# Kernel tuning notes

Measured on AMD Instinct MI355X. Metric: run time of the kernel, lower is better.

Reference implementation:

```python
import jax, jax.numpy as jnp
import numpy as np

K = 256      # embedding size k
STATE = 128  # latent state size
IN = 64      # external input size
OBS = 64     # observation size
L = 512      # sequence length (time-major)
B = 256      # batch size


def _glorot(key, shape):
    return jax.random.normal(key, shape, dtype=jnp.float32) / float(np.sqrt(shape[0]))


def setup_inputs():
    key = jax.random.key(0)
    ks = jax.random.split(key, 12)
    p = {}
    p["external_input_seq"] = jax.random.normal(ks[0], (L, B, IN), dtype=jnp.float32)
    p["observations_seq"] = jax.random.normal(ks[1], (L, B, OBS), dtype=jnp.float32)
    p["eps"] = jax.random.normal(ks[2], (L, B, STATE), dtype=jnp.float32)  # reparam noise
    # PreProcess: Linear + tanh
    p["Wu"] = _glorot(ks[3], (IN, K)); p["bu"] = jnp.zeros((K,), jnp.float32)
    p["Wx"] = _glorot(ks[4], (OBS, K)); p["bx"] = jnp.zeros((K,), jnp.float32)
    # input_rnn: vanilla tanh RNN, 1 layer, k -> k
    p["W_ih"] = _glorot(ks[5], (K, K)); p["b_ih"] = jnp.zeros((K,), jnp.float32)
    p["W_hh"] = _glorot(ks[6], (K, K)); p["b_hh"] = jnp.zeros((K,), jnp.float32)
    # posterior_a_layer: MLP(2k, k, k, 1) = Linear -> tanh -> Linear
    p["Wa1"] = _glorot(ks[7], (2 * K, K)); p["ba1"] = jnp.zeros((K,), jnp.float32)
    p["Wa2"] = _glorot(ks[8], (K, K)); p["ba2"] = jnp.zeros((K,), jnp.float32)

    def dblock_params(k1, in_dim, hid, out):
        kk = jax.random.split(k1, 4)
        return (_glorot(kk[0], (in_dim, hid)), jnp.zeros((hid,), jnp.float32),
                _glorot(kk[1], (in_dim, hid)), jnp.zeros((hid,), jnp.float32),
                _glorot(kk[2], (hid, out)), jnp.zeros((out,), jnp.float32),
                _glorot(kk[3], (hid, out)), jnp.zeros((out,), jnp.float32))

    names = ["f1_W", "f1_b", "f2_W", "f2_b", "mu_W", "mu_b", "ls_W", "ls_b"]
    for pref, kk in (("post_", ks[9]), ("prior_", ks[10])):
        vals = dblock_params(kk, STATE + K, 2 * K, STATE)
        for n, v in zip(names, vals):
            p[pref + n] = v
    return p


def _dblock(x, f1_W, f1_b, f2_W, f2_b, mu_W, mu_b, ls_W, ls_b):
    # TD-VAE DBlock: gated hidden, then mu / logsigma heads
    t = jnp.tanh(x @ f1_W + f1_b) * jax.nn.sigmoid(x @ f2_W + f2_b)
    return t @ mu_W + mu_b, t @ ls_W + ls_b


def reference(external_input_seq, observations_seq, eps, Wu, bu, Wx, bx,
              W_ih, b_ih, W_hh, b_hh, Wa1, ba1, Wa2, ba2,
              post_f1_W, post_f1_b, post_f2_W, post_f2_b, post_mu_W, post_mu_b, post_ls_W, post_ls_b,
              prior_f1_W, prior_f1_b, prior_f2_W, prior_f2_b, prior_mu_W, prior_mu_b, prior_ls_W, prior_ls_b):
    batch = external_input_seq.shape[1]
    u_emb = jnp.tanh(external_input_seq @ Wu + bu)   # [L,B,K]
    x_emb = jnp.tanh(observations_seq @ Wx + bx)     # [L,B,K]

    # input_rnn (tanh RNN) over time, d0 = 0 (memory_state=None)
    def rnn_step(d, x):
        d_new = jnp.tanh(x @ W_ih + b_ih + d @ W_hh + b_hh)
        return d_new, d_new
    d0 = jnp.zeros((batch, W_hh.shape[0]), dtype=u_emb.dtype)
    dn, d_seq = jax.lax.scan(rnn_step, d0, u_emb)    # dn [B,K], d_seq [L,B,K]

    # posterior_a_layer: pointwise MLP; flip(0) then flip(0) is a no-op for a pointwise map
    ad = jnp.concatenate([d_seq, x_emb], axis=-1)    # [L,B,2K]
    a_seq = jnp.tanh(ad @ Wa1 + ba1) @ Wa2 + ba2     # [L,B,K]

    state_size = post_mu_W.shape[1]
    z0 = jnp.zeros((batch, state_size), dtype=u_emb.dtype)

    def step(z_prev, inp):
        a_t, d_t, e_t = inp
        mean_res, logsigma = _dblock(jnp.concatenate([z_prev, a_t], axis=-1),
                                     post_f1_W, post_f1_b, post_f2_W, post_f2_b,
                                     post_mu_W, post_mu_b, post_ls_W, post_ls_b)
        prior_mean = _dblock(jnp.concatenate([z_prev, d_t], axis=-1),
                             prior_f1_W, prior_f1_b, prior_f2_W, prior_f2_b,
                             prior_mu_W, prior_mu_b, prior_ls_W, prior_ls_b)[0]
        mu = prior_mean + mean_res
        # cov = diag(exp(logsigma)) -> std = exp(0.5*logsigma); reparameterized sample
        z_new = mu + jnp.exp(0.5 * logsigma) * e_t
        return z_new, (mu, logsigma)

    zn, (state_mu, state_logsigma) = jax.lax.scan(step, z0, (a_seq, d_seq, eps))
    return state_mu, state_logsigma, dn, zn
```

## Files before the change

kernel.cpp:

```cpp
#include <hip/hip_runtime.h>

#define LSEQ 512
#define BATCH 256
#define KDIM 256
#define STATE 128

using f32x4  = __attribute__((ext_vector_type(4))) float;
using short8 = __attribute__((ext_vector_type(8))) short;
using u32x2  = __attribute__((ext_vector_type(2))) unsigned int;
using u32x4  = __attribute__((ext_vector_type(4))) unsigned int;

__device__ __forceinline__ float bf2f(unsigned short u){
  return __uint_as_float(((unsigned int)u) << 16);
}
__device__ __forceinline__ unsigned short f2bf(float f){
  unsigned int u = __float_as_uint(f);
  u += 0x7FFFu + ((u >> 16) & 1u);
  return (unsigned short)(u >> 16);
}
__device__ __forceinline__ float fast_tanh(float x){
  float ax = fabsf(x);
  float e  = __expf(2.0f * ax);
  float t  = 1.0f - 2.0f / (e + 1.0f);
  return copysignf(t, x);
}
__device__ __forceinline__ float fast_sig(float x){
  return 1.0f / (1.0f + __expf(-x));
}
__device__ __forceinline__ f32x4 mfma16(short8 a, short8 b, f32x4 c){
  return __builtin_amdgcn_mfma_f32_16x16x32_bf16(a, b, c, 0, 0, 0);
}

__device__ __forceinline__ int swz128 (int b){ return b ^ ((((b >> 7) & 7) << 4)); }
__device__ __forceinline__ int swz256 (int b){ return b ^ ((((b >> 8) & 7) << 4)); }
__device__ __forceinline__ int swz512 (int b){ return b ^ ((((b >> 9) & 7) << 4)); }

__device__ __forceinline__ void st_b128_ic(void* p, u32x4 v){
  asm volatile("global_store_dwordx4 %0, %1, off sc0 sc1" :: "v"(p), "v"(v) : "memory");
}
__device__ __forceinline__ void st_b64_ic(void* p, u32x2 v){
  asm volatile("global_store_dwordx2 %0, %1, off sc0 sc1" :: "v"(p), "v"(v) : "memory");
}
#define LD2_IC(dst, p) asm volatile("global_load_dwordx2 %0, %1, off sc0 sc1" : "=v"(dst) : "v"(p) : "memory")

__device__ __forceinline__ f32x4 cvt4(u32x2 q){
  f32x4 r;
  r[0] = __uint_as_float(q[0] << 16);
  r[1] = __uint_as_float(q[0] & 0xFFFF0000u);
  r[2] = __uint_as_float(q[1] << 16);
  r[3] = __uint_as_float(q[1] & 0xFFFF0000u);
  return r;
}

struct WDesc { const float* src; unsigned short* dst; int K, N, ld, rowoff, coloff; };
struct WDescs { WDesc d[24]; };

__global__ __launch_bounds__(256,4) void convert_weights(WDescs ds){
  WDesc w = ds.d[blockIdx.y];
  int total = w.K * w.N;
  int idx = blockIdx.x * 256 + threadIdx.x;
  if (idx < total){
    int n = idx / w.K;
    int k = idx - n * w.K;
    w.dst[idx] = f2bf(w.src[(size_t)(w.rowoff + k) * w.ld + w.coloff + n]);
  }
}

__global__ __launch_bounds__(256,1) void init_flags(int* flags){
  flags[blockIdx.x * 256 + threadIdx.x] = 0;
}

__global__ __launch_bounds__(256,4) void compose_GA(
    const float* __restrict__ Wa2, const float* __restrict__ ba2,
    const unsigned short* __restrict__ fAp,
    const float* __restrict__ pf1b, const float* __restrict__ pf2b,
    unsigned short* __restrict__ GA,
    float* __restrict__ gb)
{
  const int n = blockIdx.x;
  const int k2 = threadIdx.x;
  const unsigned short* fr = fAp + (size_t)n * 256;
  const float* wr = Wa2 + (size_t)k2 * 256;
  float s = 0.f;
  for (int j = 0; j < 256; j++) s += wr[j] * bf2f(fr[j]);
  GA[(size_t)n * 256 + k2] = f2bf(s);
  if (k2 == 0){
    float b = 0.f;
    for (int j = 0; j < 256; j++) b += ba2[j] * bf2f(fr[j]);
    gb[n] = b + ((n < 512) ? pf1b[n] : pf2b[n - 512]);
  }
}

struct GArg {
  const void* A; const unsigned short* Bt; const float* bias; const float* bias2;
  unsigned short* C; int lda, ldc, coff, K, act, a_f32;
};
struct GArgs { GArg g[4]; };

__global__ __launch_bounds__(256,2) void gemm_multi(GArgs args){
  GArg ga = args.g[blockIdx.z];
  __shared__ __align__(16) unsigned short lsA[128*64];
  __shared__ __align__(16) unsigned short lsB[128*64];
  const int tid  = threadIdx.x;
  const int wave = tid >> 6, lane = tid & 63;
  const int col_l = lane & 15, rgrp = lane >> 4;
  const int m0 = blockIdx.x * 128, n0 = blockIdx.y * 128;
  const int wm = (wave >> 1) * 64, wn = (wave & 1) * 64;

  f32x4 acc[4][4];
  const f32x4 z4 = {0.f,0.f,0.f,0.f};
  #pragma unroll
  for (int i=0;i<4;i++){ acc[i][0]=z4; acc[i][1]=z4; acc[i][2]=z4; acc[i][3]=z4; }

  const int srow = tid >> 1;
  const int sbe  = (tid & 1) * 32;

  for (int k0 = 0; k0 < ga.K; k0 += 64){
    uint4 av[4], bv[4];
    if (ga.a_f32){
      const float* Ap = (const float*)ga.A + (size_t)(m0 + srow) * ga.lda + k0 + sbe;
      uint4 fv[8];
      #pragma unroll
      for (int i=0;i<8;i++) fv[i] = *(const uint4*)((const char*)Ap + i*16);
      #pragma unroll
      for (int i=0;i<4;i++){
        const float* f = (const float*)&fv[i*2];
        uint4 o;
        o.x = (unsigned)f2bf(f[0]) | ((unsigned)f2bf(f[1]) << 16);
        o.y = (unsigned)f2bf(f[2]) | ((unsigned)f2bf(f[3]) << 16);
        o.z = (unsigned)f2bf(f[4]) | ((unsigned)f2bf(f[5]) << 16);
        o.w = (unsigned)f2bf(f[6]) | ((unsigned)f2bf(f[7]) << 16);
        av[i] = o;
      }
    } else {
      const unsigned short* Ap = (const unsigned short*)ga.A + (size_t)(m0 + srow) * ga.lda + k0 + sbe;
      #pragma unroll
      for (int i=0;i<4;i++) av[i] = *(const uint4*)((const char*)Ap + i*16);
    }
    const unsigned short* Bp = ga.Bt + (size_t)(n0 + srow) * ga.K + k0 + sbe;
    #pragma unroll
    for (int i=0;i<4;i++) bv[i] = *(const uint4*)((const char*)Bp + i*16);

    __syncthreads();
    #pragma unroll
    for (int i=0;i<4;i++){
      *(uint4*)((char*)lsA + swz128(srow*128 + sbe*2 + i*16)) = av[i];
      *(uint4*)((char*)lsB + swz128(srow*128 + sbe*2 + i*16)) = bv[i];
    }
    __syncthreads();
    #pragma unroll
    for (int kk=0; kk<2; kk++){
      short8 af[4], bfr[4];
      #pragma unroll
      for (int mt=0; mt<4; mt++)
        af[mt] = *(const short8*)((const char*)lsA + swz128((wm + mt*16 + col_l)*128 + kk*64 + rgrp*16));
      #pragma unroll
      for (int nt=0; nt<4; nt++)
        bfr[nt] = *(const short8*)((const char*)lsB + swz128((wn + nt*16 + col_l)*128 + kk*64 + rgrp*16));
      #pragma unroll
      for (int mt=0; mt<4; mt++)
        #pragma unroll
        for (int nt=0; nt<4; nt++)
          acc[mt][nt] = mfma16(af[mt], bfr[nt], acc[mt][nt]);
    }
  }
  #pragma unroll
  for (int nt=0; nt<4; nt++){
    int col = n0 + wn + nt*16 + col_l;
    const float* bsrc = (col < 512) ? ga.bias : ga.bias2;
    float bb = bsrc ? bsrc[col & 511] : 0.0f;
    #pragma unroll
    for (int mt=0; mt<4; mt++){
      #pragma unroll
      for (int r=0; r<4; r++){
        int row = m0 + wm + mt*16 + rgrp*4 + r;
        float v = acc[mt][nt][r] + bb;
        if (ga.act == 1) v = fast_tanh(v);
        ga.C[(size_t)row * ga.ldc + ga.coff + col] = f2bf(v);
      }
    }
  }
}

struct GArg2 {
  const unsigned short* A; const unsigned short* Bt; const float* bias; const float* bias2;
  unsigned short* C; int lda, ldc, coff, K, act;
};
struct GArgs2 { GArg2 g[2]; };

__global__ __launch_bounds__(256,2) void gemm_glds(GArgs2 args){
  GArg2 ga = args.g[blockIdx.z];
  __shared__ __align__(16) unsigned short ls[4][128*64];
  const int tid  = threadIdx.x;
  const int wave = tid >> 6, lane = tid & 63;
  const int col_l = lane & 15, rgrp = lane >> 4;
  const int m0 = blockIdx.x * 128, n0 = blockIdx.y * 128;
  const int wm = (wave >> 1) * 64, wn = (wave & 1) * 64;

  const int lrow = lane >> 3;
  const int scol = (((lane & 7) ^ lrow) << 3);

  auto STAGE = [&](int k0, int buf){
    #pragma unroll
    for (int c = 0; c < 4; c++){
      int srow = wave*32 + c*8 + lrow;
      const unsigned short* pa = ga.A  + (size_t)(m0 + srow) * ga.lda + k0 + scol;
      const unsigned short* pb = ga.Bt + (size_t)(n0 + srow) * ga.K  + k0 + scol;
      __builtin_amdgcn_global_load_lds(
          (const __attribute__((address_space(1))) unsigned int*)pa,
          (__attribute__((address_space(3))) unsigned int*)((char*)&ls[buf*2][0]   + wave*4096 + c*1024),
          16, 0, 0);
      __builtin_amdgcn_global_load_lds(
          (const __attribute__((address_space(1))) unsigned int*)pb,
          (__attribute__((address_space(3))) unsigned int*)((char*)&ls[buf*2+1][0] + wave*4096 + c*1024),
          16, 0, 0);
    }
  };

  f32x4 acc[4][4];
  const f32x4 z4 = {0.f,0.f,0.f,0.f};
  #pragma unroll
  for (int i=0;i<4;i++){ acc[i][0]=z4; acc[i][1]=z4; acc[i][2]=z4; acc[i][3]=z4; }

  const int niter = ga.K >> 6;
  STAGE(0, 0);

  for (int i = 0; i < niter; i++){
    if (i + 1 < niter){
      STAGE((i+1)*64, (i+1) & 1);
      asm volatile("s_waitcnt vmcnt(8)" ::: "memory");
    } else {
      asm volatile("s_waitcnt vmcnt(0)" ::: "memory");
    }
    __syncthreads();
    const char* la = (const char*)&ls[(i&1)*2][0];
    const char* lb = (const char*)&ls[(i&1)*2+1][0];
    #pragma unroll
    for (int kk=0; kk<2; kk++){
      short8 af[4], bfr[4];
      #pragma unroll
      for (int mt=0; mt<4; mt++)
        af[mt] = *(const short8*)(la + swz128((wm + mt*16 + col_l)*128 + kk*64 + rgrp*16));
      #pragma unroll
      for (int nt=0; nt<4; nt++)
        bfr[nt] = *(const short8*)(lb + swz128((wn + nt*16 + col_l)*128 + kk*64 + rgrp*16));
      #pragma unroll
      for (int mt=0; mt<4; mt++)
        #pragma unroll
        for (int nt=0; nt<4; nt++)
          acc[mt][nt] = mfma16(af[mt], bfr[nt], acc[mt][nt]);
    }
    __syncthreads();
  }

  #pragma unroll
  for (int nt=0; nt<4; nt++){
    int col = n0 + wn + nt*16 + col_l;
    const float* bsrc = (col < 512) ? ga.bias : ga.bias2;
    float bb = bsrc ? bsrc[col & 511] : 0.0f;
    #pragma unroll
    for (int mt=0; mt<4; mt++){
      #pragma unroll
      for (int r=0; r<4; r++){
        int row = m0 + wm + mt*16 + rgrp*4 + r;
        float v = acc[mt][nt][r] + bb;
        if (ga.act == 1) v = fast_tanh(v);
        ga.C[(size_t)row * ga.ldc + ga.coff + col] = f2bf(v);
      }
    }
  }
}

__global__ __launch_bounds__(256,1) void rnn_chunk(
    const unsigned short* __restrict__ rnn_in,
    const unsigned short* __restrict__ Whh_t,
    const float* __restrict__ b_hh,
    unsigned short* __restrict__ cat_d,
    float* __restrict__ dn_out,
    unsigned short* __restrict__ d_state,
    int t0, int nsteps)
{
  __shared__ __align__(16) unsigned short dls[16*256];
  const int tid = threadIdx.x, wave = tid >> 6, lane = tid & 63;
  const int col_l = lane & 15, rgrp = lane >> 4;
  const int brow0 = blockIdx.x * 16;
  const int ncol = wave * 64;

  short8 bfr[4][8];
  #pragma unroll
  for (int nt=0; nt<4; nt++){
    const unsigned short* bp = Whh_t + (size_t)(ncol + nt*16 + col_l) * 256;
    #pragma unroll
    for (int kk=0; kk<8; kk++)
      bfr[nt][kk] = *(const short8*)(bp + kk*32 + rgrp*8);
  }
  float bias[4];
  #pragma unroll
  for (int nt=0; nt<4; nt++) bias[nt] = b_hh[ncol + nt*16 + col_l];

  if (t0 == 0){
    for (int i = tid; i < 16*256; i += 256){
      int row = i >> 8, col = i & 255;
      *(unsigned short*)((char*)dls + swz512(row*512 + col*2)) = 0;
    }
  } else {
    const unsigned short* ds = d_state + (size_t)brow0 * 256;
    for (int i = tid; i < 16*256; i += 256){
      int row = i >> 8, col = i & 255;
      *(unsigned short*)((char*)dls + swz512(row*512 + col*2)) = ds[row*256 + col];
    }
  }
  __syncthreads();

  for (int tl=0; tl<nsteps; tl++){
    unsigned short rv[4][4];
    const unsigned short* rp = rnn_in + (size_t)(tl*BATCH + brow0) * 256;
    #pragma unroll
    for (int nt=0; nt<4; nt++)
      #pragma unroll
      for (int r=0; r<4; r++)
        rv[nt][r] = rp[(size_t)(rgrp*4 + r)*256 + ncol + nt*16 + col_l];

    f32x4 acc[4];
    const f32x4 z4 = {0.f,0.f,0.f,0.f};
    acc[0]=z4; acc[1]=z4; acc[2]=z4; acc[3]=z4;
    #pragma unroll
    for (int kk=0; kk<8; kk++){
      short8 af = *(const short8*)((const char*)dls + swz512((lane & 15)*512 + kk*64 + rgrp*16));
      #pragma unroll
      for (int nt=0; nt<4; nt++)
        acc[nt] = mfma16(af, bfr[nt][kk], acc[nt]);
    }
    __syncthreads();
    #pragma unroll
    for (int nt=0; nt<4; nt++){
      #pragma unroll
      for (int r=0; r<4; r++){
        float h = acc[nt][r] + bf2f(rv[nt][r]) + bias[nt];
        float d = fast_tanh(h);
        int row = rgrp*4 + r, col = ncol + nt*16 + col_l;
        unsigned short db = f2bf(d);
        *(unsigned short*)((char*)dls + swz512(row*512 + col*2)) = db;
        cat_d[(size_t)(tl*BATCH + brow0 + row)*512 + col] = db;
        if (t0 + tl == LSEQ-1) dn_out[(size_t)(brow0 + row)*256 + col] = d;
      }
    }
    __syncthreads();
  }
  unsigned short* dso = d_state + (size_t)brow0 * 256;
  for (int i = tid; i < 16*256; i += 256){
    int row = i >> 8, col = i & 255;
    dso[row*256 + col] = *(const unsigned short*)((const char*)dls + swz512(row*512 + col*2));
  }
}

__global__ __launch_bounds__(512,1) void zrec_mb(
    const unsigned short* __restrict__ preP, const unsigned short* __restrict__ preQ,
    const unsigned short* __restrict__ Wzz,
    const unsigned short* __restrict__ W2,
    const float* __restrict__ pmub, const float* __restrict__ plsb, const float* __restrict__ qmub,
    const float* __restrict__ eps,
    float* __restrict__ out_mu, float* __restrict__ out_ls, float* __restrict__ out_zn,
    unsigned short* __restrict__ z_state,
    unsigned short* __restrict__ mb, int* __restrict__ flags,
    int t0, int nsteps, int fbase)
{
  __shared__ __align__(16) unsigned short zls[16*128];
  __shared__ __align__(16) unsigned short tls[16*256];
  __shared__ __align__(16) unsigned short bls[16*256];
  const int tid = threadIdx.x, wave = tid >> 6, lane = tid & 63;
  const int col_l = lane & 15, rgrp = lane >> 4;
  const int bid = blockIdx.x;
  const int c   = (bid >> 3) & 3;
  const int g   = (bid & 7) + ((bid >> 5) << 3);
  const int brow0 = g * 16;
  const int NT2 = (c < 2) ? 2 : 1;

  const unsigned short* pre = (c < 2) ? preP : preQ;
  const int cb = (c & 1) * 256;

  short8 w1[2][2][4];
  {
    const unsigned short* wz = Wzz + (size_t)c * 65536;
    #pragma unroll
    for (int m=0; m<2; m++)
      #pragma unroll
      for (int nt=0; nt<2; nt++){
        int n = wave*32 + nt*16 + col_l;
        #pragma unroll
        for (int kk=0; kk<4; kk++)
          w1[m][nt][kk] = *(const short8*)(wz + (size_t)(m*256 + n)*128 + kk*32 + rgrp*8);
      }
  }
  short8 w2r[2][8];
  {
    const unsigned short* wp = W2 + (size_t)c * 65536;
    #pragma unroll
    for (int nt=0; nt<2; nt++){
      if (nt < NT2){
        int ccol = wave*(16*((c<2)?2:1)) + nt*16;
        int mat = (c < 2) ? (ccol >> 7) : 0;
        int n   = (ccol & 127) + col_l;
        #pragma unroll
        for (int kk=0; kk<8; kk++)
          w2r[nt][kk] = *(const short8*)(wp + (size_t)(mat*128 + n)*256 + kk*32 + rgrp*8);
      }
    }
  }
  int* const fline  = flags + g*32;
  int* const myflag = fline + c;

  if (t0 == 0){
    for (int i = tid; i < 16*128; i += 512){
      int row = i >> 7, col = i & 127;
      *(unsigned short*)((char*)zls + swz256(row*256 + col*2)) = 0;
    }
  } else {
    const unsigned short* zs = z_state + (size_t)brow0 * 128;
    for (int i = tid; i < 16*128; i += 512){
      int row = i >> 7, col = i & 127;
      *(unsigned short*)((char*)zls + swz256(row*256 + col*2)) = zs[row*128 + col];
    }
  }
  __syncthreads();

  auto LD_PRE = [&](int tl, unsigned short (&pa_)[2][4], unsigned short (&pb_)[2][4]){
    const unsigned short* bA = pre + ((size_t)tl*BATCH + brow0)*1024 + cb;
    #pragma unroll
    for (int nt=0; nt<2; nt++)
      #pragma unroll
      for (int r=0; r<4; r++){
        int row = rgrp*4 + r, col = wave*32 + nt*16 + col_l;
        pa_[nt][r] = bA[(size_t)row*1024 + col];
        pb_[nt][r] = bA[(size_t)row*1024 + 512 + col];
      }
  };

  const int rrow = tid >> 5;
  const int rc0  = (tid & 31) * 4;
  const f32x4 bp4 = *(const f32x4*)(pmub + rc0);
  const f32x4 bl4 = *(const f32x4*)(plsb + rc0);
  const f32x4 bq4 = *(const f32x4*)(qmub + rc0);

  unsigned short pa0[2][4], pb0[2][4], pa1[2][4], pb1[2][4];
  LD_PRE(0, pa0, pb0);

  const f32x4 z4 = {0.f,0.f,0.f,0.f};
  for (int tl=0; tl<nsteps; ++tl){
    size_t growr = (size_t)(t0+tl)*BATCH + brow0 + rrow;
    f32x4 er = *(const f32x4*)(eps + growr*STATE + rc0);
    int nx = (tl+1 < nsteps) ? tl+1 : tl;
    LD_PRE(nx, pa1, pb1);

    short8 af1[4];
    #pragma unroll
    for (int kk=0; kk<4; kk++)
      af1[kk] = *(const short8*)((const char*)zls + swz256((lane & 15)*256 + kk*64 + rgrp*16));
    f32x4 a1[2][2];
    a1[0][0]=z4; a1[0][1]=z4; a1[1][0]=z4; a1[1][1]=z4;
    #pragma unroll
    for (int kk=0; kk<4; kk++)
      #pragma unroll
      for (int m=0; m<2; m++)
        #pragma unroll
        for (int nt=0; nt<2; nt++)
          a1[m][nt] = mfma16(af1[kk], w1[m][nt][kk], a1[m][nt]);

    #pragma unroll
    for (int nt=0; nt<2; nt++)
      #pragma unroll
      for (int r=0; r<4; r++){
        float h1 = a1[0][nt][r] + bf2f(pa0[nt][r]);
        float h2 = a1[1][nt][r] + bf2f(pb0[nt][r]);
        float tv = fast_tanh(h1) * fast_sig(h2);
        int row = rgrp*4 + r, tcol = wave*32 + nt*16 + col_l;
        *(unsigned short*)((char*)tls + swz512(row*512 + tcol*2)) = f2bf(tv);
      }
    __syncthreads();

    f32x4 a2[2];
    a2[0]=z4; a2[1]=z4;
    #pragma unroll
    for (int kk=0; kk<8; kk++){
      short8 af2 = *(const short8*)((const char*)tls + swz512((lane & 15)*512 + kk*64 + rgrp*16));
      #pragma unroll
      for (int nt=0; nt<2; nt++)
        if (nt < NT2) a2[nt] = mfma16(af2, w2r[nt][kk], a2[nt]);
    }
    if (c < 2){
      #pragma unroll
      for (int nt=0; nt<2; nt++)
        #pragma unroll
        for (int r=0; r<4; r++)
          bls[(rgrp*4 + r)*256 + wave*32 + nt*16 + col_l] = f2bf(a2[nt][r]);
    } else {
      #pragma unroll
      for (int r=0; r<4; r++)
        bls[(rgrp*4 + r)*128 + wave*16 + col_l] = f2bf(a2[0][r]);
    }
    __syncthreads();

    unsigned short* slot = mb + (size_t)((g*2 + (tl & 1))*4 + c)*4096;
    if (c < 2){
      u32x4 v = *(const u32x4*)((const char*)bls + tid*16);
      st_b128_ic(slot + tid*8, v);
    } else {
      u32x2 v = *(const u32x2*)((const char*)bls + tid*8);
      st_b64_ic(slot + tid*4, v);
    }
    asm volatile("s_waitcnt vmcnt(0)" ::: "memory");
    __syncthreads();
    const int target = fbase + tl + 1;
    if (tid == 0)
      __hip_atomic_store(myflag, target, __ATOMIC_RELAXED, __HIP_MEMORY_SCOPE_AGENT);

    if (lane == 0){
      u32x4 F;
      for (;;){
        asm volatile("global_load_dwordx4 %0, %1, off sc0 sc1\n\ts_waitcnt vmcnt(0)"
                     : "=v"(F) : "v"(fline) : "memory");
        int ok = 1;
        #pragma unroll
        for (int p=0; p<4; p++)
          if (p != c && (int)F[p] < target) ok = 0;
        if (ok) break;
        __builtin_amdgcn_s_sleep(1);
      }
    }

    const unsigned short* mbb = mb + (size_t)((g*2 + (tl & 1))*4)*4096;
    const unsigned short* s0 = mbb;
    const unsigned short* s1 = mbb + 4096;
    const unsigned short* s2 = mbb + 8192;
    const unsigned short* s3 = mbb + 12288;
    u32x2 q0,q1,q2,q3,q4,q5;
    LD2_IC(q0, s0 + rrow*256 + rc0);
    LD2_IC(q1, s1 + rrow*256 + rc0);
    LD2_IC(q2, s0 + rrow*256 + 128 + rc0);
    LD2_IC(q3, s1 + rrow*256 + 128 + rc0);
    LD2_IC(q4, s2 + rrow*128 + rc0);
    LD2_IC(q5, s3 + rrow*128 + rc0);
    asm volatile("s_waitcnt vmcnt(0)" ::: "memory");
    __builtin_amdgcn_sched_barrier(0);

    f32x4 mup = cvt4(q0) + cvt4(q1);
    f32x4 lsv = cvt4(q2) + cvt4(q3) + bl4;
    f32x4 muq = cvt4(q4) + cvt4(q5);
    f32x4 muv = (muq + bq4) + (mup + bp4);
    f32x4 zv;
    #pragma unroll
    for (int i=0; i<4; i++) zv[i] = muv[i] + __expf(0.5f * lsv[i]) * er[i];

    unsigned int lo = (unsigned)f2bf(zv[0]) | ((unsigned)f2bf(zv[1]) << 16);
    unsigned int hi = (unsigned)f2bf(zv[2]) | ((unsigned)f2bf(zv[3]) << 16);
    uint2 zp; zp.x = lo; zp.y = hi;
    *(uint2*)((char*)zls + swz256(rrow*256 + rc0*2)) = zp;
    if (c == 0){
      *(f32x4*)(out_mu + growr*STATE + rc0) = muv;
      *(f32x4*)(out_ls + growr*STATE + rc0) = lsv;
      if (t0 + tl == LSEQ-1)
        *(f32x4*)(out_zn + ((size_t)(brow0 + rrow))*STATE + rc0) = zv;
    }
    __syncthreads();

    #pragma unroll
    for (int nt=0; nt<2; nt++)
      #pragma unroll
      for (int r=0; r<4; r++){ pa0[nt][r] = pa1[nt][r]; pb0[nt][r] = pb1[nt][r]; }
  }

  if (c == 0){
    unsigned short* zso = z_state + (size_t)brow0 * 128;
    for (int i = tid; i < 16*128; i += 512){
      int row = i >> 7, col = i & 127;
      zso[row*128 + col] = *(const unsigned short*)((const char*)zls + swz256(row*256 + col*2));
    }
  }
}

extern "C" void kernel_launch(void* const* d_in, const int* in_sizes, int n_in,
                              void* d_out, int out_size, void* d_ws, size_t ws_size,
                              hipStream_t stream)
{
  const float* ext = (const float*)d_in[0];
  const float* obs = (const float*)d_in[1];
  const float* eps = (const float*)d_in[2];
  const float* Wu  = (const float*)d_in[3];
  const float* bu  = (const float*)d_in[4];
  const float* Wx  = (const float*)d_in[5];
  const float* bx  = (const float*)d_in[6];
  const float* W_ih= (const float*)d_in[7];
  const float* b_ih= (const float*)d_in[8];
  const float* W_hh= (const float*)d_in[9];
  const float* b_hh= (const float*)d_in[10];
  const float* Wa1 = (const float*)d_in[11];
  const float* ba1 = (const float*)d_in[12];
  const float* Wa2 = (const float*)d_in[13];
  const float* ba2 = (const float*)d_in[14];
  const float* pf1W= (const float*)d_in[15]; const float* pf1b = (const float*)d_in[16];
  const float* pf2W= (const float*)d_in[17]; const float* pf2b = (const float*)d_in[18];
  const float* pmuW= (const float*)d_in[19]; const float* pmub = (const float*)d_in[20];
  const float* plsW= (const float*)d_in[21]; const float* plsb = (const float*)d_in[22];
  const float* qf1W= (const float*)d_in[23]; const float* qf1b = (const float*)d_in[24];
  const float* qf2W= (const float*)d_in[25]; const float* qf2b = (const float*)d_in[26];
  const float* qmuW= (const float*)d_in[27]; const float* qmub = (const float*)d_in[28];

  int NC = 0;
  const int cands[7] = {1,2,4,8,16,32,64};
  size_t rows = 0;
  for (int ci=0; ci<7; ci++){
    size_t r = (size_t)(LSEQ/cands[ci])*BATCH;
    size_t elems = 3400000 + r*3072;
    if (elems * 2 <= ws_size){ NC = cands[ci]; rows = r; break; }
  }
  if (!NC) return;
  const int nsteps = LSEQ/NC;
  const int gx = (int)(rows/128);

  unsigned short* ws = (unsigned short*)d_ws;
  size_t off = 0;
  auto alloc = [&](size_t elems){
    unsigned short* p = ws + off;
    off += (elems + 127) & ~(size_t)127;
    return p;
  };

  unsigned short* Wu_t  = alloc(64*256);
  unsigned short* Wx_t  = alloc(64*256);
  unsigned short* Wih_t = alloc(256*256);
  unsigned short* Whh_t = alloc(256*256);
  unsigned short* Wa1_t = alloc(512*256);
  unsigned short* Wa2_t = alloc(256*256);
  unsigned short* fAp   = alloc(1024*256);
  unsigned short* fAq   = alloc(1024*256);
  unsigned short* GAp   = alloc(1024*256);
  float*          gbp   = (float*)alloc(2048);
  unsigned short* Wzz   = alloc(4*2*256*128);
  unsigned short* W2z   = alloc(4*2*128*256);
  unsigned short* d_state = alloc(256*256);
  unsigned short* z_state = alloc(256*128);
  unsigned short* mbx  = alloc(16*2*4*4096);
  int*   flg  = (int*)alloc(4096);
  unsigned short* bufA  = alloc(rows*256);
  unsigned short* bufB  = alloc(rows*256);
  unsigned short* bufC  = alloc(rows*512);
  unsigned short* preP  = alloc(rows*1024);
  unsigned short* preQ  = alloc(rows*1024);
  if (off * sizeof(unsigned short) > ws_size) return;

  float* out_mu = (float*)d_out;
  float* out_ls = out_mu + (size_t)LSEQ*BATCH*STATE;
  float* out_dn = out_ls + (size_t)LSEQ*BATCH*STATE;
  float* out_zn = out_dn + (size_t)BATCH*KDIM;

  WDescs wd;
  int wi = 0;
  auto add = [&](const float* s, unsigned short* d, int Kk, int Nn, int ld, int ro, int co){
    wd.d[wi].src = s; wd.d[wi].dst = d; wd.d[wi].K = Kk; wd.d[wi].N = Nn;
    wd.d[wi].ld = ld; wd.d[wi].rowoff = ro; wd.d[wi].coloff = co; wi++;
  };
  add(Wu,   Wu_t,  64, 256, 256, 0, 0);
  add(Wx,   Wx_t,  64, 256, 256, 0, 0);
  add(W_ih, Wih_t, 256, 256, 256, 0, 0);
  add(W_hh, Whh_t, 256, 256, 256, 0, 0);
  add(Wa1,  Wa1_t, 512, 256, 256, 0, 0);
  add(Wa2,  Wa2_t, 256, 256, 256, 0, 0);
  add(pf1W, fAp,            256, 512, 512, 128, 0);
  add(pf2W, fAp + 512*256,  256, 512, 512, 128, 0);
  add(qf1W, fAq,            256, 512, 512, 128, 0);
  add(qf2W, fAq + 512*256,  256, 512, 512, 128, 0);
  for (int c=0; c<4; c++){
    const float* s1 = (c < 2) ? pf1W : qf1W;
    const float* s2 = (c < 2) ? pf2W : qf2W;
    add(s1, Wzz + (size_t)(c*2+0)*32768, 128, 256, 512, 0, (c&1)*256);
    add(s2, Wzz + (size_t)(c*2+1)*32768, 128, 256, 512, 0, (c&1)*256);
  }
  add(pmuW, W2z + (size_t)(0*2+0)*32768, 256, 128, 128, 0,   0);
  add(plsW, W2z + (size_t)(0*2+1)*32768, 256, 128, 128, 0,   0);
  add(pmuW, W2z + (size_t)(1*2+0)*32768, 256, 128, 128, 256, 0);
  add(plsW, W2z + (size_t)(1*2+1)*32768, 256, 128, 128, 256, 0);
  add(qmuW, W2z + (size_t)(2*2+0)*32768, 256, 128, 128, 0,   0);
  add(qmuW, W2z + (size_t)(3*2+0)*32768, 256, 128, 128, 256, 0);

  convert_weights<<<dim3(512,24), 256, 0, stream>>>(wd);
  compose_GA<<<1024, 256, 0, stream>>>(Wa2, ba2, fAp, pf1b, pf2b, GAp, gbp);
  init_flags<<<8, 256, 0, stream>>>(flg);

  for (int c=0; c<NC; ++c){
    const int t0 = c * nsteps;
    const size_t row0 = (size_t)t0 * BATCH;

    GArgs e{};
    e.g[0] = GArg{ext + row0*64, Wu_t, bu, bu, bufA, 64, 256, 0,   64, 1, 1};
    e.g[1] = GArg{obs + row0*64, Wx_t, bx, bx, bufC, 64, 512, 256, 64, 1, 1};
    gemm_multi<<<dim3(gx,2,2), 256, 0, stream>>>(e);

    GArgs2 rn{};
    rn.g[0] = GArg2{bufA, Wih_t, b_ih, b_ih, bufB, 256, 256, 0, 256, 0};
    gemm_glds<<<dim3(gx,2,1), 256, 0, stream>>>(rn);

    rnn_chunk<<<16, 256, 0, stream>>>(bufB, Whh_t, b_hh, bufC, out_dn, d_state, t0, nsteps);

    GArgs2 a1{};
    a1.g[0] = GArg2{bufC, Wa1_t, ba1, ba1, bufA, 512, 256, 0, 512, 1};
    gemm_glds<<<dim3(gx,2,1), 256, 0, stream>>>(a1);

    GArgs2 pr{};
    pr.g[0] = GArg2{bufA, GAp, gbp, gbp + 512, preP, 256, 1024, 0, 256, 0};
    pr.g[1] = GArg2{bufC, fAq, qf1b, qf2b, preQ, 512, 1024, 0, 256, 0};
    gemm_glds<<<dim3(gx,8,2), 256, 0, stream>>>(pr);

    zrec_mb<<<64, 512, 0, stream>>>(preP, preQ, Wzz, W2z,
                                    pmub, plsb, qmub, eps, out_mu, out_ls, out_zn,
                                    z_state, mbx, flg, t0, nsteps, c*nsteps);
  }
}
```

Baseline: 3.630 ms.

## Overlap z-recurrence of previous chunk with next chunk's GEMM/RNN stages in megakernel

Merges the GEMM, RNN and z-recurrence kernels into one launch, where 64 blocks run a segment of the previous chunk's z-recurrence while the remaining blocks run one stage of the current chunk's pipeline. The pre-activation buffers are double-buffered by chunk parity, and the recurrence is split into five segments across the five stages. The aim is to hide the latency-bound serial recurrence behind the parallel GEMM work. In exchange it uses more workspace and 512-thread blocks with 128KB of shared memory, which lowers GEMM occupancy. It also relies on co-resident blocks for the flag-based recurrence sync.

After: 3.517 ms. -3.1%, faster.

```diff
diff --git a/kernel.cpp b/kernel.cpp
--- a/kernel.cpp
+++ b/kernel.cpp
@@ -74,8 +74,7 @@
     const float* __restrict__ Wa2, const float* __restrict__ ba2,
     const unsigned short* __restrict__ fAp,
     const float* __restrict__ pf1b, const float* __restrict__ pf2b,
-    unsigned short* __restrict__ GA,
-    float* __restrict__ gb)
+    unsigned short* __restrict__ GA, float* __restrict__ gb)
 {
   const int n = blockIdx.x;
   const int k2 = threadIdx.x;
@@ -95,16 +94,17 @@
   const void* A; const unsigned short* Bt; const float* bias; const float* bias2;
   unsigned short* C; int lda, ldc, coff, K, act, a_f32;
 };
-struct GArgs { GArg g[4]; };
-
-__global__ __launch_bounds__(256,2) void gemm_multi(GArgs args){
-  GArg ga = args.g[blockIdx.z];
-  __shared__ __align__(16) unsigned short lsA[128*64];
-  __shared__ __align__(16) unsigned short lsB[128*64];
-  const int tid  = threadIdx.x;
+struct GArg2 {
+  const unsigned short* A; const unsigned short* Bt; const float* bias; const float* bias2;
+  unsigned short* C; int lda, ldc, coff, K, act;
+};
+
+__device__ void gemm_multi_body(const GArg ga, int bx, int by, int tid, char* lsraw){
+  char* lsA = lsraw;
+  char* lsB = lsraw + 16384;
   const int wave = tid >> 6, lane = tid & 63;
   const int col_l = lane & 15, rgrp = lane >> 4;
-  const int m0 = blockIdx.x * 128, n0 = blockIdx.y * 128;
+  const int m0 = bx * 128, n0 = by * 128;
   const int wm = (wave >> 1) * 64, wn = (wave & 1) * 64;
 
   f32x4 acc[4][4];
@@ -144,8 +144,8 @@
     __syncthreads();
     #pragma unroll
     for (int i=0;i<4;i++){
-      *(uint4*)((char*)lsA + swz128(srow*128 + sbe*2 + i*16)) = av[i];
-      *(uint4*)((char*)lsB + swz128(srow*128 + sbe*2 + i*16)) = bv[i];
+      *(uint4*)(lsA + swz128(srow*128 + sbe*2 + i*16)) = av[i];
+      *(uint4*)(lsB + swz128(srow*128 + sbe*2 + i*16)) = bv[i];
     }
     __syncthreads();
     #pragma unroll
@@ -153,10 +153,10 @@
       short8 af[4], bfr[4];
       #pragma unroll
       for (int mt=0; mt<4; mt++)
-        af[mt] = *(const short8*)((const char*)lsA + swz128((wm + mt*16 + col_l)*128 + kk*64 + rgrp*16));
+        af[mt] = *(const short8*)(lsA + swz128((wm + mt*16 + col_l)*128 + kk*64 + rgrp*16));
       #pragma unroll
       for (int nt=0; nt<4; nt++)
-        bfr[nt] = *(const short8*)((const char*)lsB + swz128((wn + nt*16 + col_l)*128 + kk*64 + rgrp*16));
+        bfr[nt] = *(const short8*)(lsB + swz128((wn + nt*16 + col_l)*128 + kk*64 + rgrp*16));
       #pragma unroll
       for (int mt=0; mt<4; mt++)
         #pragma unroll
@@ -182,19 +182,10 @@
   }
 }
 
-struct GArg2 {
-  const unsigned short* A; const unsigned short* Bt; const float* bias; const float* bias2;
-  unsigned short* C; int lda, ldc, coff, K, act;
-};
-struct GArgs2 { GArg2 g[2]; };
-
-__global__ __launch_bounds__(256,2) void gemm_glds(GArgs2 args){
-  GArg2 ga = args.g[blockIdx.z];
-  __shared__ __align__(16) unsigned short ls[4][128*64];
-  const int tid  = threadIdx.x;
+__device__ void gemm_glds_body(const GArg2 ga, int bx, int by, int tid, char* lsraw){
   const int wave = tid >> 6, lane = tid & 63;
   const int col_l = lane & 15, rgrp = lane >> 4;
-  const int m0 = blockIdx.x * 128, n0 = blockIdx.y * 128;
+  const int m0 = bx * 128, n0 = by * 128;
   const int wm = (wave >> 1) * 64, wn = (wave & 1) * 64;
 
   const int lrow = lane >> 3;
@@ -208,11 +199,11 @@
       const unsigned short* pb = ga.Bt + (size_t)(n0 + srow) * ga.K  + k0 + scol;
       __builtin_amdgcn_global_load_lds(
           (const __attribute__((address_space(1))) unsigned int*)pa,
-          (__attribute__((address_space(3))) unsigned int*)((char*)&ls[buf*2][0]   + wave*4096 + c*1024),
+          (__attribute__((address_space(3))) unsigned int*)(lsraw + buf*32768 + wave*4096 + c*1024),
           16, 0, 0);
       __builtin_amdgcn_global_load_lds(
           (const __attribute__((address_space(1))) unsigned int*)pb,
-          (__attribute__((address_space(3))) unsigned int*)((char*)&ls[buf*2+1][0] + wave*4096 + c*1024),
+          (__attribute__((address_space(3))) unsigned int*)(lsraw + buf*32768 + 16384 + wave*4096 + c*1024),
           16, 0, 0);
     }
   };
@@ -233,8 +224,8 @@
       asm volatile("s_waitcnt vmcnt(0)" ::: "memory");
     }
     __syncthreads();
-    const char* la = (const char*)&ls[(i&1)*2][0];
-    const char* lb = (const char*)&ls[(i&1)*2+1][0];
+    const char* la = lsraw + (i&1)*32768;
+    const char* lb = la + 16384;
     #pragma unroll
     for (int kk=0; kk<2; kk++){
       short8 af[4], bfr[4];
@@ -271,19 +262,15 @@
   }
 }
 
-__global__ __launch_bounds__(256,1) void rnn_chunk(
-    const unsigned short* __restrict__ rnn_in,
-    const unsigned short* __restrict__ Whh_t,
-    const float* __restrict__ b_hh,
-    unsigned short* __restrict__ cat_d,
-    float* __restrict__ dn_out,
-    unsigned short* __restrict__ d_state,
-    int t0, int nsteps)
+__device__ void rnn_body(
+    const unsigned short* rnn_in, const unsigned short* Whh_t, const float* b_hh,
+    unsigned short* cat_d, float* dn_out, unsigned short* d_state,
+    int t0, int nsteps, int bx, int tid, char* lsraw)
 {
-  __shared__ __align__(16) unsigned short dls[16*256];
-  const int tid = threadIdx.x, wave = tid >> 6, lane = tid & 63;
+  char* dls = lsraw;
+  const int wave = tid >> 6, lane = tid & 63;
   const int col_l = lane & 15, rgrp = lane >> 4;
-  const int brow0 = blockIdx.x * 16;
+  const int brow0 = bx * 16;
   const int ncol = wave * 64;
 
   short8 bfr[4][8];
@@ -301,13 +288,13 @@
   if (t0 == 0){
     for (int i = tid; i < 16*256; i += 256){
       int row = i >> 8, col = i & 255;
-      *(unsigned short*)((char*)dls + swz512(row*512 + col*2)) = 0;
+      *(unsigned short*)(dls + swz512(row*512 + col*2)) = 0;
     }
   } else {
     const unsigned short* ds = d_state + (size_t)brow0 * 256;
     for (int i = tid; i < 16*256; i += 256){
       int row = i >> 8, col = i & 255;
-      *(unsigned short*)((char*)dls + swz512(row*512 + col*2)) = ds[row*256 + col];
+      *(unsigned short*)(dls + swz512(row*512 + col*2)) = ds[row*256 + col];
     }
   }
   __syncthreads();
@@ -326,7 +313,7 @@
     acc[0]=z4; acc[1]=z4; acc[2]=z4; acc[3]=z4;
     #pragma unroll
     for (int kk=0; kk<8; kk++){
-      short8 af = *(const short8*)((const char*)dls + swz512((lane & 15)*512 + kk*64 + rgrp*16));
+      short8 af = *(const short8*)(dls + swz512((lane & 15)*512 + kk*64 + rgrp*16));
       #pragma unroll
       for (int nt=0; nt<4; nt++)
         acc[nt] = mfma16(af, bfr[nt][kk], acc[nt]);
@@ -340,7 +327,7 @@
         float d = fast_tanh(h);
         int row = rgrp*4 + r, col = ncol + nt*16 + col_l;
         unsigned short db = f2bf(d);
-        *(unsigned short*)((char*)dls + swz512(row*512 + col*2)) = db;
+        *(unsigned short*)(dls + swz512(row*512 + col*2)) = db;
         cat_d[(size_t)(tl*BATCH + brow0 + row)*512 + col] = db;
         if (t0 + tl == LSEQ-1) dn_out[(size_t)(brow0 + row)*256 + col] = d;
       }
@@ -350,27 +337,23 @@
   unsigned short* dso = d_state + (size_t)brow0 * 256;
   for (int i = tid; i < 16*256; i += 256){
     int row = i >> 8, col = i & 255;
-    dso[row*256 + col] = *(const unsigned short*)((const char*)dls + swz512(row*512 + col*2));
-  }
-}
-
-__global__ __launch_bounds__(512,1) void zrec_mb(
-    const unsigned short* __restrict__ preP, const unsigned short* __restrict__ preQ,
-    const unsigned short* __restrict__ Wzz,
-    const unsigned short* __restrict__ W2,
-    const float* __restrict__ pmub, const float* __restrict__ plsb, const float* __restrict__ qmub,
-    const float* __restrict__ eps,
-    float* __restrict__ out_mu, float* __restrict__ out_ls, float* __restrict__ out_zn,
-    unsigned short* __restrict__ z_state,
-    unsigned short* __restrict__ mb, int* __restrict__ flags,
-    int t0, int nsteps, int fbase)
+    dso[row*256 + col] = *(const unsigned short*)(dls + swz512(row*512 + col*2));
+  }
+}
+
+__device__ void zrec_body(
+    const unsigned short* preP, const unsigned short* preQ,
+    const unsigned short* Wzz, const unsigned short* W2,
+    const float* pmub, const float* plsb, const float* qmub,
+    const float* eps, float* out_mu, float* out_ls, float* out_zn,
+    unsigned short* z_state, unsigned short* mb, int* flags,
+    int t0, int nsteps, int poff, int bid, int tid, char* lsraw)
 {
-  __shared__ __align__(16) unsigned short zls[16*128];
-  __shared__ __align__(16) unsigned short tls[16*256];
-  __shared__ __align__(16) unsigned short bls[16*256];
-  const int tid = threadIdx.x, wave = tid >> 6, lane = tid & 63;
+  unsigned short* zls = (unsigned short*)lsraw;
+  unsigned short* tls = (unsigned short*)(lsraw + 4096);
+  unsigned short* bls = (unsigned short*)(lsraw + 12288);
+  const int wave = tid >> 6, lane = tid & 63;
   const int col_l = lane & 15, rgrp = lane >> 4;
-  const int bid = blockIdx.x;
   const int c   = (bid >> 3) & 3;
   const int g   = (bid & 7) + ((bid >> 5) << 3);
   const int brow0 = g * 16;
@@ -425,7 +408,7 @@
   __syncthreads();
 
   auto LD_PRE = [&](int tl, unsigned short (&pa_)[2][4], unsigned short (&pb_)[2][4]){
-    const unsigned short* bA = pre + ((size_t)tl*BATCH + brow0)*1024 + cb;
+    const unsigned short* bA = pre + ((size_t)(poff + tl)*BATCH + brow0)*1024 + cb;
     #pragma unroll
     for (int nt=0; nt<2; nt++)
       #pragma unroll
@@ -451,6 +434,7 @@
     f32x4 er = *(const f32x4*)(eps + growr*STATE + rc0);
     int nx = (tl+1 < nsteps) ? tl+1 : tl;
     LD_PRE(nx, pa1, pb1);
+    const int par = (t0 + tl) & 1;
 
     short8 af1[4];
     #pragma unroll
@@ -500,7 +484,7 @@
     }
     __syncthreads();
 
-    unsigned short* slot = mb + (size_t)((g*2 + (tl & 1))*4 + c)*4096;
+    unsigned short* slot = mb + (size_t)((g*2 + par)*4 + c)*4096;
     if (c < 2){
       u32x4 v = *(const u32x4*)((const char*)bls + tid*16);
       st_b128_ic(slot + tid*8, v);
@@ -510,7 +494,7 @@
     }
     asm volatile("s_waitcnt vmcnt(0)" ::: "memory");
     __syncthreads();
-    const int target = fbase + tl + 1;
+    const int target = t0 + tl + 1;
     if (tid == 0)
       __hip_atomic_store(myflag, target, __ATOMIC_RELAXED, __HIP_MEMORY_SCOPE_AGENT);
 
@@ -528,7 +512,7 @@
       }
     }
 
-    const unsigned short* mbb = mb + (size_t)((g*2 + (tl & 1))*4)*4096;
+    const unsigned short* mbb = mb + (size_t)((g*2 + par)*4)*4096;
     const unsigned short* s0 = mbb;
     const unsigned short* s1 = mbb + 4096;
     const unsigned short* s2 = mbb + 8192;
@@ -575,6 +559,47 @@
       int row = i >> 7, col = i & 127;
       zso[row*128 + col] = *(const unsigned short*)((const char*)zls + swz256(row*256 + col*2));
     }
+  }
+}
+
+struct MegaArgs {
+  const unsigned short *zP, *zQ, *Wzz, *W2;
+  const float *pmub, *plsb, *qmub, *eps;
+  float *out_mu, *out_ls, *out_zn;
+  unsigned short *zst, *mb; int *flags;
+  int t0z, nsz, poff;
+  int stage, gx;
+  GArg  e0, e1;
+  GArg2 p0, p1;
+  const unsigned short *rnn_in, *Whh; const float* b_hh;
+  unsigned short* cat_d; float* dn_out; unsigned short* dstt; int t0r, nsr;
+};
+
+__global__ __launch_bounds__(512,1) void mega(MegaArgs A){
+  __shared__ __align__(16) char smem[131072];
+  const int tid = threadIdx.x;
+  if ((int)blockIdx.x < 64){
+    if (A.nsz > 0)
+      zrec_body(A.zP, A.zQ, A.Wzz, A.W2, A.pmub, A.plsb, A.qmub, A.eps,
+                A.out_mu, A.out_ls, A.out_zn, A.zst, A.mb, A.flags,
+                A.t0z, A.nsz, A.poff, (int)blockIdx.x, tid, smem);
+    return;
+  }
+  const int pb = (int)blockIdx.x - 64;
+  const int half = tid >> 8, ltid = tid & 255;
+  char* ls = smem + half*65536;
+  const int lg = pb*2 + half;
+  if (A.stage == 0){
+    int bxx = lg % A.gx, t = lg / A.gx;
+    gemm_multi_body((t >= 2) ? A.e1 : A.e0, bxx, t & 1, ltid, ls);
+  } else if (A.stage == 1 || A.stage == 3){
+    int bxx = lg % A.gx, by = lg / A.gx;
+    gemm_glds_body(A.p0, bxx, by, ltid, ls);
+  } else if (A.stage == 2){
+    rnn_body(A.rnn_in, A.Whh, A.b_hh, A.cat_d, A.dn_out, A.dstt, A.t0r, A.nsr, lg, ltid, ls);
+  } else if (A.stage == 4){
+    int bxx = lg % A.gx, t = lg / A.gx;
+    gemm_glds_body((t >> 3) ? A.p1 : A.p0, bxx, t & 7, ltid, ls);
   }
 }
 
@@ -606,11 +631,11 @@
   const float* qmuW= (const float*)d_in[27]; const float* qmub = (const float*)d_in[28];
 
   int NC = 0;
-  const int cands[7] = {1,2,4,8,16,32,64};
+  const int cands[5] = {4,8,16,32,64};
   size_t rows = 0;
-  for (int ci=0; ci<7; ci++){
+  for (int ci=0; ci<5; ci++){
     size_t r = (size_t)(LSEQ/cands[ci])*BATCH;
-    size_t elems = 3400000 + r*3072;
+    size_t elems = 2600000 + r*5120;
     if (elems * 2 <= ws_size){ NC = cands[ci]; rows = r; break; }
   }
   if (!NC) return;
@@ -630,7 +655,6 @@
   unsigned short* Wih_t = alloc(256*256);
   unsigned short* Whh_t = alloc(256*256);
   unsigned short* Wa1_t = alloc(512*256);
-  unsigned short* Wa2_t = alloc(256*256);
   unsigned short* fAp   = alloc(1024*256);
   unsigned short* fAq   = alloc(1024*256);
   unsigned short* GAp   = alloc(1024*256);
@@ -644,8 +668,10 @@
   unsigned short* bufA  = alloc(rows*256);
   unsigned short* bufB  = alloc(rows*256);
   unsigned short* bufC  = alloc(rows*512);
-  unsigned short* preP  = alloc(rows*1024);
-  unsigned short* preQ  = alloc(rows*1024);
+  unsigned short* preP0 = alloc(rows*1024);
+  unsigned short* preP1 = alloc(rows*1024);
+  unsigned short* preQ0 = alloc(rows*1024);
+  unsigned short* preQ1 = alloc(rows*1024);
   if (off * sizeof(unsigned short) > ws_size) return;
 
   float* out_mu = (float*)d_out;
@@ -664,7 +690,6 @@
   add(W_ih, Wih_t, 256, 256, 256, 0, 0);
   add(W_hh, Whh_t, 256, 256, 256, 0, 0);
   add(Wa1,  Wa1_t, 512, 256, 256, 0, 0);
-  add(Wa2,  Wa2_t, 256, 256, 256, 0, 0);
   add(pf1W, fAp,            256, 512, 512, 128, 0);
   add(pf2W, fAp + 512*256,  256, 512, 512, 128, 0);
   add(qf1W, fAq,            256, 512, 512, 128, 0);
@@ -682,36 +707,62 @@
   add(qmuW, W2z + (size_t)(2*2+0)*32768, 256, 128, 128, 0,   0);
   add(qmuW, W2z + (size_t)(3*2+0)*32768, 256, 128, 128, 256, 0);
 
-  convert_weights<<<dim3(512,24), 256, 0, stream>>>(wd);
+  convert_weights<<<dim3(512, wi), 256, 0, stream>>>(wd);
   compose_GA<<<1024, 256, 0, stream>>>(Wa2, ba2, fAp, pf1b, pf2b, GAp, gbp);
   init_flags<<<8, 256, 0, stream>>>(flg);
 
+  int s4 = (nsteps/5) & ~1;
+  int segs[5] = {s4, s4, s4, s4, nsteps - 4*s4};
+
+  auto zfill = [&](MegaArgs& A, int c_z){
+    A.zP = (c_z & 1) ? preP1 : preP0;
+    A.zQ = (c_z & 1) ? preQ1 : preQ0;
+    A.Wzz = Wzz; A.W2 = W2z; A.pmub = pmub; A.plsb = plsb; A.qmub = qmub;
+    A.eps = eps; A.out_mu = out_mu; A.out_ls = out_ls; A.out_zn = out_zn;
+    A.zst = z_state; A.mb = mbx; A.flags = flg;
+  };
+
   for (int c=0; c<NC; ++c){
-    const int t0 = c * nsteps;
-    const size_t row0 = (size_t)t0 * BATCH;
-
-    GArgs e{};
-    e.g[0] = GArg{ext + row0*64, Wu_t, bu, bu, bufA, 64, 256, 0,   64, 1, 1};
-    e.g[1] = GArg{obs + row0*64, Wx_t, bx, bx, bufC, 64, 512, 256, 64, 1, 1};
-    gemm_multi<<<dim3(gx,2,2), 256, 0, stream>>>(e);
-
-    GArgs2 rn{};
-    rn.g[0] = GArg2{bufA, Wih_t, b_ih, b_ih, bufB, 256, 256, 0, 256, 0};
-    gemm_glds<<<dim3(gx,2,1), 256, 0, stream>>>(rn);
-
-    rnn_chunk<<<16, 256, 0, stream>>>(bufB, Whh_t, b_hh, bufC, out_dn, d_state, t0, nsteps);
-
-    GArgs2 a1{};
-    a1.g[0] = GArg2{bufC, Wa1_t, ba1, ba1, bufA, 512, 256, 0, 512, 1};
-    gemm_glds<<<dim3(gx,2,1), 256, 0, stream>>>(a1);
-
-    GArgs2 pr{};
-    pr.g[0] = GArg2{bufA, GAp, gbp, gbp + 512, preP, 256, 1024, 0, 256, 0};
-    pr.g[1] = GArg2{bufC, fAq, qf1b, qf2b, preQ, 512, 1024, 0, 256, 0};
-    gemm_glds<<<dim3(gx,8,2), 256, 0, stream>>>(pr);
-
-    zrec_mb<<<64, 512, 0, stream>>>(preP, preQ, Wzz, W2z,
-                                    pmub, plsb, qmub, eps, out_mu, out_ls, out_zn,
-                                    z_state, mbx, flg, t0, nsteps, c*nsteps);
-  }
-}
+    const size_t row0 = (size_t)c * nsteps * BATCH;
+    unsigned short* pP = (c & 1) ? preP1 : preP0;
+    unsigned short* pQ = (c & 1) ? preQ1 : preQ0;
+    int zo = 0;
+    for (int st=0; st<5; st++){
+      MegaArgs A{};
+      zfill(A, c-1);
+      A.t0z = (c-1)*nsteps + zo;
+      A.poff = zo;
+      A.nsz = (c == 0) ? 0 : segs[st];
+      zo += segs[st];
+      A.stage = st; A.gx = gx;
+      int nphys;
+      if (st == 0){
+        A.e0 = GArg{ext + row0*64, Wu_t, bu, bu, bufA, 64, 256, 0,   64, 1, 1};
+        A.e1 = GArg{obs + row0*64, Wx_t, bx, bx, bufC, 64, 512, 256, 64, 1, 1};
+        nphys = gx*2;
+      } else if (st == 1){
+        A.p0 = GArg2{bufA, Wih_t, b_ih, b_ih, bufB, 256, 256, 0, 256, 0};
+        nphys = gx;
+      } else if (st == 2){
+        A.rnn_in = bufB; A.Whh = Whh_t; A.b_hh = b_hh; A.cat_d = bufC;
+        A.dn_out = out_dn; A.dstt = d_state; A.t0r = c*nsteps; A.nsr = nsteps;
+        nphys = 8;
+      } else if (st == 3){
+        A.p0 = GArg2{bufC, Wa1_t, ba1, ba1, bufA, 512, 256, 0, 512, 1};
+        nphys = gx;
+      } else {
+        A.p0 = GArg2{bufA, GAp, gbp, gbp + 512, pP, 256, 1024, 0, 256, 0};
+        A.p1 = GArg2{bufC, fAq, qf1b, qf2b, pQ, 512, 1024, 0, 256, 0};
+        nphys = gx*8;
+      }
+      mega<<<64 + nphys, 512, 0, stream>>>(A);
+    }
+  }
+  {
+    MegaArgs A{};
+    zfill(A, NC-1);
+    A.t0z = (NC-1)*nsteps; A.poff = 0; A.nsz = nsteps;
+    A.stage = 5; A.gx = gx;
+    mega<<<64, 512, 0, stream>>>(A);
+  }
+}
```
